# Performance work log

Hardware: AMD Instinct MI355X
Metric: run time of the kernel (lower is better)

## Reference

```python
import jax, jax.numpy as jnp
import numpy as np

B, S, D, H = 4, 2048, 1024, 16
DK = D // H


def setup_inputs() -> dict:
    key = jax.random.key(0)
    ks = jax.random.split(key, 12)
    scale = 1.0 / np.sqrt(D)
    inp = {
        'q': jax.random.normal(ks[0], (B, S, D), jnp.float32),
        'k': jax.random.normal(ks[1], (B, S, D), jnp.float32),
        'v': jax.random.normal(ks[2], (B, S, D), jnp.float32),
        'mask': jnp.ones((1, 1, S, S), jnp.int32),
        'wq': jax.random.normal(ks[3], (D, D), jnp.float32) * scale,
        'bq': jnp.zeros((D,), jnp.float32),
        'wk': jax.random.normal(ks[4], (D, D), jnp.float32) * scale,
        'bk': jnp.zeros((D,), jnp.float32),
        'wv': jax.random.normal(ks[5], (D, D), jnp.float32) * scale,
        'bv': jnp.zeros((D,), jnp.float32),
        'wo': jax.random.normal(ks[6], (D, D), jnp.float32) * scale,
        'bo': jnp.zeros((D,), jnp.float32),
    }
    return inp


def reference(q, k, v, mask, wq, bq, wk, bk, wv, bv, wo, bo):
    # torch Linear: y = x @ W^T + b
    def proj(x, w, b):
        return jnp.einsum('bsd,ed->bse', x, w) + b

    # [B,S,D] -> [B,H,S,DK]
    def split_heads(x):
        return x.reshape(B, S, H, DK).transpose(0, 2, 1, 3)

    query = split_heads(proj(q, wq, bq))
    key_ = split_heads(proj(k, wk, bk))
    value = split_heads(proj(v, wv, bv))

    scores = jnp.einsum('bhqd,bhkd->bhqk', query, key_) / jnp.sqrt(jnp.float32(DK))
    scores = jnp.where(mask == 0, jnp.float32(-1e9), scores)
    attn = jax.nn.softmax(scores, axis=-1)  # dropout p=0 (eval): identity
    x = jnp.einsum('bhqk,bhkd->bhqd', attn, value)
    x = x.transpose(0, 2, 1, 3).reshape(B, S, D)
    return jnp.einsum('bsd,ed->bse', x, wo) + bo
```

## Files before the change

### kernel.cpp

```cpp
#include <hip/hip_runtime.h>
#include <hip/hip_bf16.h>
#include <cstdint>
#include <cstddef>


typedef __attribute__((ext_vector_type(4))) float f32x4;
typedef __attribute__((ext_vector_type(8))) short s16x8;
typedef __attribute__((ext_vector_type(4))) short s16x4;
typedef __attribute__((ext_vector_type(8))) unsigned short u16x8;
typedef __attribute__((ext_vector_type(4))) unsigned short u16x4;
typedef __attribute__((ext_vector_type(2))) unsigned u32x2;

#define AS1 __attribute__((address_space(1)))
#define AS3 __attribute__((address_space(3)))

__device__ __forceinline__ unsigned short f2bf(float f) {
  unsigned u = __builtin_bit_cast(unsigned, f);
  u += 0x7fffu + ((u >> 16) & 1u);
  return (unsigned short)(u >> 16);
}

__device__ __forceinline__ void gload16(const void* g, void* l) {
  __builtin_amdgcn_global_load_lds((const AS1 unsigned*)g, (AS3 unsigned*)l, 16, 0, 0);
}

__device__ __forceinline__ float exp2_fast(float x) {
  float r; asm("v_exp_f32 %0, %1" : "=v"(r) : "v"(x)); return r;
}
__device__ __forceinline__ float max3f(float a, float b, float c) {
  float d; asm("v_max3_f32 %0, %1, %2, %3" : "=v"(d) : "v"(a), "v"(b), "v"(c)); return d;
}
__device__ __forceinline__ unsigned cvt_pk_bf16(float lo, float hi) {
  unsigned r; asm("v_cvt_pk_bf16_f32 %0, %1, %2" : "=v"(r) : "v"(lo), "v"(hi)); return r;
}

__global__ __launch_bounds__(256) void cvt_f32_bf16(const float* __restrict__ in,
                                                    unsigned short* __restrict__ out,
                                                    int n8) {
  int i = blockIdx.x * 256 + threadIdx.x;
  if (i >= n8) return;
  const f32x4* p = (const f32x4*)in;
  f32x4 a = p[2 * i], b = p[2 * i + 1];
  u16x8 o;
  o[0] = f2bf(a[0]); o[1] = f2bf(a[1]); o[2] = f2bf(a[2]); o[3] = f2bf(a[3]);
  o[4] = f2bf(b[0]); o[5] = f2bf(b[1]); o[6] = f2bf(b[2]); o[7] = f2bf(b[3]);
  *(u16x8*)(out + (size_t)i * 8) = o;
}

__global__ __launch_bounds__(256) void cvt_w4(const float* __restrict__ w0,
                                              const float* __restrict__ w1,
                                              const float* __restrict__ w2,
                                              const float* __restrict__ w3,
                                              unsigned short* __restrict__ out) {
  int y = blockIdx.y;
  const float* src = (y == 0) ? w0 : (y == 1) ? w1 : (y == 2) ? w2 : w3;
  int i = blockIdx.x * 256 + threadIdx.x;
  if (i >= 131072) return;
  const f32x4* p = (const f32x4*)src;
  f32x4 a = p[2 * i], b = p[2 * i + 1];
  u16x8 o;
  o[0] = f2bf(a[0]); o[1] = f2bf(a[1]); o[2] = f2bf(a[2]); o[3] = f2bf(a[3]);
  o[4] = f2bf(b[0]); o[5] = f2bf(b[1]); o[6] = f2bf(b[2]); o[7] = f2bf(b[3]);
  *(u16x8*)(out + (size_t)y * 1048576 + (size_t)i * 8) = o;
}

template <int MODE>
__global__ __launch_bounds__(256) void gemm_bt(const unsigned short* __restrict__ A,
                                               const unsigned short* __restrict__ W,
                                               const float* __restrict__ bias,
                                               float oscale,
                                               void* __restrict__ outp) {
  __shared__ char lds[32768];
  const int tid = threadIdx.x;
  const int w = tid >> 6, lane = tid & 63, c = lane & 15, g = lane >> 4;
  const int wr = w >> 1, wc = w & 1;
  const int tm = blockIdx.x, tn = blockIdx.y;

  f32x4 acc[4][4] = {};
  const char* Abase = (const char*)A + ((size_t)tm * 128) * 2048;
  const char* Bbase = (const char*)W + ((size_t)tn * 128) * 2048;

  for (int kt = 0; kt < 16; ++kt) {
    if (kt) __syncthreads();
#pragma unroll
    for (int j = 0; j < 4; ++j) {
      int slotb = (j * 4 + w) * 64;
      int slot = slotb + lane;
      int row = slot >> 3;
      int c16 = (slot & 7) ^ (row & 7);
      gload16(Abase + (size_t)row * 2048 + kt * 128 + c16 * 16, lds + slotb * 16);
    }
#pragma unroll
    for (int j = 0; j < 4; ++j) {
      int slotb = (j * 4 + w) * 64;
      int slot = slotb + lane;
      int row = slot >> 3;
      int c16 = (slot & 7) ^ (row & 7);
      gload16(Bbase + (size_t)row * 2048 + kt * 128 + c16 * 16, lds + 16384 + slotb * 16);
    }
    asm volatile("s_waitcnt vmcnt(0)" ::: "memory");
    __syncthreads();

#pragma unroll
    for (int ks = 0; ks < 2; ++ks) {
      s16x8 af[4], bfr[4];
#pragma unroll
      for (int mi = 0; mi < 4; ++mi) {
        int row = wr * 64 + mi * 16 + c;
        af[mi] = *(const s16x8*)(lds + row * 128 + ((ks * 64 + g * 16) ^ ((row & 7) << 4)));
      }
#pragma unroll
      for (int ni = 0; ni < 4; ++ni) {
        int row = wc * 64 + ni * 16 + c;
        bfr[ni] = *(const s16x8*)(lds + 16384 + row * 128 + ((ks * 64 + g * 16) ^ ((row & 7) << 4)));
      }
#pragma unroll
      for (int mi = 0; mi < 4; ++mi)
#pragma unroll
        for (int ni = 0; ni < 4; ++ni)
          acc[mi][ni] = __builtin_amdgcn_mfma_f32_16x16x32_bf16(af[mi], bfr[ni], acc[mi][ni], 0, 0, 0);
    }
  }

  int col[4];
  float bv[4];
#pragma unroll
  for (int ni = 0; ni < 4; ++ni) {
    col[ni] = tn * 128 + wc * 64 + ni * 16 + c;
    bv[ni] = bias[col[ni]];
  }

  if constexpr (MODE == 2) {
    float* out = (float*)outp;
#pragma unroll
    for (int mi = 0; mi < 4; ++mi) {
      int row0 = tm * 128 + wr * 64 + mi * 16 + g * 4;
#pragma unroll
      for (int ni = 0; ni < 4; ++ni)
#pragma unroll
        for (int r = 0; r < 4; ++r)
          out[(size_t)(row0 + r) * 1024 + col[ni]] = acc[mi][ni][r] + bv[ni];
    }
  } else if constexpr (MODE == 0) {
    unsigned short* out = (unsigned short*)outp;
#pragma unroll
    for (int mi = 0; mi < 4; ++mi) {
      int row0 = tm * 128 + wr * 64 + mi * 16 + g * 4;
#pragma unroll
      for (int ni = 0; ni < 4; ++ni)
#pragma unroll
        for (int r = 0; r < 4; ++r)
          out[(size_t)(row0 + r) * 1024 + col[ni]] = f2bf((acc[mi][ni][r] + bv[ni]) * oscale);
    }
  } else {
    unsigned short* Vt = (unsigned short*)outp;
#pragma unroll
    for (int mi = 0; mi < 4; ++mi) {
      int m0 = tm * 128 + wr * 64 + mi * 16 + g * 4;
      int b = m0 >> 11, s = m0 & 2047;
#pragma unroll
      for (int ni = 0; ni < 4; ++ni) {
        u16x4 pk;
#pragma unroll
        for (int r = 0; r < 4; ++r) pk[r] = f2bf(acc[mi][ni][r] + bv[ni]);
        *(u16x4*)(Vt + ((size_t)(b * 1024 + col[ni])) * 2048 + s) = pk;
      }
    }
  }
}

__global__ __launch_bounds__(256) void attn_kernel(const unsigned short* __restrict__ Q,
                                                   const unsigned short* __restrict__ K,
                                                   const unsigned short* __restrict__ Vt,
                                                   unsigned short* __restrict__ X) {
  __shared__ char lds[32768];
  const int tid = threadIdx.x, w = tid >> 6, lane = tid & 63, c = lane & 15, g = lane >> 4;
  const int qt = blockIdx.x, bh = blockIdx.y, b = bh >> 4;
  const size_t qkbase = ((size_t)b * 2048) * 1024 + (size_t)(bh & 15) * 64;
  const int q0 = qt * 64 + w * 16;

  s16x8 qf[2];
  {
    const unsigned short* qp = Q + qkbase + (size_t)(q0 + c) * 1024;
    qf[0] = *(const s16x8*)(qp + g * 8);
    qf[1] = *(const s16x8*)(qp + 32 + g * 8);
  }

  const int row0 = w * 8 + (lane >> 3);
  const int c16 = (lane & 7) ^ (lane >> 3);
  const int sb0 = w * 1024, sb1 = 4096 + w * 1024;
  const char* kb0 = (const char*)(K + qkbase) + (size_t)row0 * 2048 + c16 * 16;
  const char* kb1 = kb0 + 32 * 2048;
  const char* vb0 = (const char*)Vt + ((size_t)bh * 64 + row0) * 4096 + c16 * 16;
  const char* vb1 = vb0 + 32 * 4096;

  const int M = (c & 7) << 4;
  const int koff0 = (g * 16) ^ M, koff1 = (64 + g * 16) ^ M;
  int voff[4];
#pragma unroll
  for (int mt = 0; mt < 4; ++mt) voff[mt] = (mt * 32 + g * 8) ^ M;

  auto stage = [&](int half, int kt) {
    char* dst = (char*)lds + half * 16384;
    gload16(kb0 + (size_t)kt * 131072, dst + sb0);
    gload16(kb1 + (size_t)kt * 131072, dst + sb1);
    gload16(vb0 + (size_t)kt * 128, dst + 8192 + sb0);
    gload16(vb1 + (size_t)kt * 128, dst + 8192 + sb1);
  };

  f32x4 acc_o[4] = {};
  float m_run = -INFINITY, l_run = 0.f;

  stage(0, 0);

  for (int kt = 0; kt < 32; ++kt) {
    const int cur = kt & 1;
    asm volatile("s_waitcnt vmcnt(0)" ::: "memory");
    __syncthreads();
    if (kt + 1 < 32) stage(cur ^ 1, kt + 1);

    const char* kr = (const char*)lds + cur * 16384 + c * 128;
    const char* vr = kr + 8192;

    f32x4 s4[4] = {};
    __builtin_amdgcn_s_setprio(1);
#pragma unroll
    for (int mt = 0; mt < 4; ++mt) {
      s16x8 kf = *(const s16x8*)(kr + mt * 2048 + koff0);
      s4[mt] = __builtin_amdgcn_mfma_f32_16x16x32_bf16(kf, qf[0], s4[mt], 0, 0, 0);
    }
#pragma unroll
    for (int mt = 0; mt < 4; ++mt) {
      s16x8 kf = *(const s16x8*)(kr + mt * 2048 + koff1);
      s4[mt] = __builtin_amdgcn_mfma_f32_16x16x32_bf16(kf, qf[1], s4[mt], 0, 0, 0);
    }
    __builtin_amdgcn_s_setprio(0);

    float t[16];
#pragma unroll
    for (int mt = 0; mt < 4; ++mt)
#pragma unroll
      for (int r = 0; r < 4; ++r) t[mt * 4 + r] = s4[mt][r];

    float a0 = max3f(t[0], t[1], t[2]);
    float a1 = max3f(t[3], t[4], t[5]);
    float a2 = max3f(t[6], t[7], t[8]);
    float a3 = max3f(t[9], t[10], t[11]);
    float a4 = max3f(t[12], t[13], t[14]);
    float mx = fmaxf(max3f(a0, a1, a2), max3f(a3, a4, t[15]));
    mx = fmaxf(mx, __shfl_xor(mx, 16));
    mx = fmaxf(mx, __shfl_xor(mx, 32));

    if (!__all(mx <= m_run + 8.f)) {
      float m_new = fmaxf(m_run, mx);
      float alpha = exp2_fast(m_run - m_new);
      float al[4];
#pragma unroll
      for (int r = 0; r < 4; ++r) al[r] = __shfl(alpha, (lane & 48) + g * 4 + r);
#pragma unroll
      for (int nc = 0; nc < 4; ++nc)
#pragma unroll
        for (int r = 0; r < 4; ++r) acc_o[nc][r] *= al[r];
      l_run *= alpha;
      m_run = m_new;
    }

    float p[16];
#pragma unroll
    for (int i = 0; i < 16; ++i) p[i] = exp2_fast(t[i] - m_run);
    float r0 = (p[0] + p[1]) + (p[2] + p[3]);
    float r1 = (p[4] + p[5]) + (p[6] + p[7]);
    float r2 = (p[8] + p[9]) + (p[10] + p[11]);
    float r3 = (p[12] + p[13]) + (p[14] + p[15]);
    float rs = (r0 + r1) + (r2 + r3);
    rs += __shfl_xor(rs, 16);
    rs += __shfl_xor(rs, 32);
    l_run += rs;

    s16x4 pf[4];
#pragma unroll
    for (int mt = 0; mt < 4; ++mt) {
      u32x2 pk;
      pk[0] = cvt_pk_bf16(p[mt * 4 + 0], p[mt * 4 + 1]);
      pk[1] = cvt_pk_bf16(p[mt * 4 + 2], p[mt * 4 + 3]);
      pf[mt] = __builtin_bit_cast(s16x4, pk);
    }

    __builtin_amdgcn_s_setprio(1);
#pragma unroll
    for (int mt = 0; mt < 4; ++mt) {
#pragma unroll
      for (int nc = 0; nc < 4; ++nc) {
        s16x4 vf = *(const s16x4*)(vr + nc * 2048 + voff[mt]);
        acc_o[nc] = __builtin_amdgcn_mfma_f32_16x16x16bf16_1k(pf[mt], vf, acc_o[nc], 0, 0, 0);
      }
    }
    __builtin_amdgcn_s_setprio(0);
  }

  float linv = 1.f / l_run;
  float li[4];
#pragma unroll
  for (int r = 0; r < 4; ++r) li[r] = __shfl(linv, (lane & 48) + g * 4 + r);
#pragma unroll
  for (int nc = 0; nc < 4; ++nc)
#pragma unroll
    for (int r = 0; r < 4; ++r)
      X[qkbase + (size_t)(q0 + g * 4 + r) * 1024 + nc * 16 + c] = f2bf(acc_o[nc][r] * li[r]);
}

extern "C" void kernel_launch(void* const* d_in, const int* in_sizes, int n_in,
                              void* d_out, int out_size, void* d_ws, size_t ws_size,
                              hipStream_t stream) {
  const float* q  = (const float*)d_in[0];
  const float* k  = (const float*)d_in[1];
  const float* v  = (const float*)d_in[2];
  const float* wq = (const float*)d_in[4];
  const float* bq = (const float*)d_in[5];
  const float* wk = (const float*)d_in[6];
  const float* bk = (const float*)d_in[7];
  const float* wv = (const float*)d_in[8];
  const float* bv = (const float*)d_in[9];
  const float* wo = (const float*)d_in[10];
  const float* bo = (const float*)d_in[11];

  char* ws = (char*)d_ws;
  unsigned short* buf = (unsigned short*)ws;
  unsigned short* wb  = (unsigned short*)(ws + (size_t)16777216);
  unsigned short* Vt  = (unsigned short*)(ws + (size_t)25165824);

  unsigned short* Qb = (unsigned short*)d_out;
  unsigned short* Kb = Qb + 8388608;

  const float qscale = 0.18033688011112042f;

  cvt_w4<<<dim3(512, 4), 256, 0, stream>>>(wq, wk, wv, wo, wb);

  cvt_f32_bf16<<<4096, 256, 0, stream>>>(q, buf, 1048576);
  gemm_bt<0><<<dim3(64, 8), 256, 0, stream>>>(buf, wb + 0,       bq, qscale, (void*)Qb);
  cvt_f32_bf16<<<4096, 256, 0, stream>>>(k, buf, 1048576);
  gemm_bt<0><<<dim3(64, 8), 256, 0, stream>>>(buf, wb + 1048576, bk, 1.0f, (void*)Kb);
  cvt_f32_bf16<<<4096, 256, 0, stream>>>(v, buf, 1048576);
  gemm_bt<1><<<dim3(64, 8), 256, 0, stream>>>(buf, wb + 2097152, bv, 1.0f, (void*)Vt);

  attn_kernel<<<dim3(32, 64), 256, 0, stream>>>(Qb, Kb, Vt, buf);

  gemm_bt<2><<<dim3(64, 8), 256, 0, stream>>>(buf, wb + 3145728, bo, 1.0f, d_out);
}
```

Baseline: 401.1 us.

## Double-buffer GEMM LDS, process two query tiles per attention wave, permute V layout

The GEMM now double-buffers its LDS tiles (64KB), prefetching the next K-slice while computing the current one, and raises wave priority around its MFMA bursts. The attention kernel has each wave handle 32 query rows as two 16-row sub-tiles, so every K/V fragment read from LDS feeds twice as many MFMAs, and the grid is halved to match. The V-transpose store is permuted within 64-element groups so attention can read V as 16-byte vectors and split them into halves. The cost is higher register and LDS pressure, which may lower occupancy, and fewer attention blocks overall.

Measured after the change: 394.4 us. No clear change (-1.7%).

```diff
diff --git a/kernel.cpp b/kernel.cpp
--- a/kernel.cpp
+++ b/kernel.cpp
@@ -70,7 +70,7 @@
                                                const float* __restrict__ bias,
                                                float oscale,
                                                void* __restrict__ outp) {
-  __shared__ char lds[32768];
+  __shared__ char lds[65536];
   const int tid = threadIdx.x;
   const int w = tid >> 6, lane = tid & 63, c = lane & 15, g = lane >> 4;
   const int wr = w >> 1, wc = w & 1;
@@ -80,45 +80,48 @@
   const char* Abase = (const char*)A + ((size_t)tm * 128) * 2048;
   const char* Bbase = (const char*)W + ((size_t)tn * 128) * 2048;
 
-  for (int kt = 0; kt < 16; ++kt) {
-    if (kt) __syncthreads();
+  auto stage = [&](int half, int kt) {
+    char* dst = (char*)lds + half * 32768;
 #pragma unroll
     for (int j = 0; j < 4; ++j) {
       int slotb = (j * 4 + w) * 64;
       int slot = slotb + lane;
       int row = slot >> 3;
       int c16 = (slot & 7) ^ (row & 7);
-      gload16(Abase + (size_t)row * 2048 + kt * 128 + c16 * 16, lds + slotb * 16);
-    }
-#pragma unroll
-    for (int j = 0; j < 4; ++j) {
-      int slotb = (j * 4 + w) * 64;
-      int slot = slotb + lane;
-      int row = slot >> 3;
-      int c16 = (slot & 7) ^ (row & 7);
-      gload16(Bbase + (size_t)row * 2048 + kt * 128 + c16 * 16, lds + 16384 + slotb * 16);
-    }
+      gload16(Abase + (size_t)row * 2048 + kt * 128 + c16 * 16, dst + slotb * 16);
+      gload16(Bbase + (size_t)row * 2048 + kt * 128 + c16 * 16, dst + 16384 + slotb * 16);
+    }
+  };
+
+  stage(0, 0);
+
+  for (int kt = 0; kt < 16; ++kt) {
+    const int cur = kt & 1;
     asm volatile("s_waitcnt vmcnt(0)" ::: "memory");
     __syncthreads();
-
+    if (kt + 1 < 16) stage(cur ^ 1, kt + 1);
+
+    const char* base = (const char*)lds + cur * 32768;
 #pragma unroll
     for (int ks = 0; ks < 2; ++ks) {
       s16x8 af[4], bfr[4];
 #pragma unroll
       for (int mi = 0; mi < 4; ++mi) {
         int row = wr * 64 + mi * 16 + c;
-        af[mi] = *(const s16x8*)(lds + row * 128 + ((ks * 64 + g * 16) ^ ((row & 7) << 4)));
+        af[mi] = *(const s16x8*)(base + row * 128 + ((ks * 64 + g * 16) ^ ((row & 7) << 4)));
       }
 #pragma unroll
       for (int ni = 0; ni < 4; ++ni) {
         int row = wc * 64 + ni * 16 + c;
-        bfr[ni] = *(const s16x8*)(lds + 16384 + row * 128 + ((ks * 64 + g * 16) ^ ((row & 7) << 4)));
-      }
+        bfr[ni] = *(const s16x8*)(base + 16384 + row * 128 + ((ks * 64 + g * 16) ^ ((row & 7) << 4)));
+      }
+      __builtin_amdgcn_s_setprio(1);
 #pragma unroll
       for (int mi = 0; mi < 4; ++mi)
 #pragma unroll
         for (int ni = 0; ni < 4; ++ni)
           acc[mi][ni] = __builtin_amdgcn_mfma_f32_16x16x32_bf16(af[mi], bfr[ni], acc[mi][ni], 0, 0, 0);
+      __builtin_amdgcn_s_setprio(0);
     }
   }
 
@@ -158,12 +161,15 @@
     for (int mi = 0; mi < 4; ++mi) {
       int m0 = tm * 128 + wr * 64 + mi * 16 + g * 4;
       int b = m0 >> 11, s = m0 & 2047;
+      int sl = s & 63;
+      int mt_l = sl >> 4, gg = (sl >> 2) & 3;
+      int npos = ((mt_l >> 1) << 5) + gg * 8 + ((mt_l & 1) << 2);
 #pragma unroll
       for (int ni = 0; ni < 4; ++ni) {
         u16x4 pk;
 #pragma unroll
         for (int r = 0; r < 4; ++r) pk[r] = f2bf(acc[mi][ni][r] + bv[ni]);
-        *(u16x4*)(Vt + ((size_t)(b * 1024 + col[ni])) * 2048 + s) = pk;
+        *(u16x4*)(Vt + ((size_t)(b * 1024 + col[ni])) * 2048 + (s & ~63) + npos) = pk;
       }
     }
   }
@@ -177,13 +183,16 @@
   const int tid = threadIdx.x, w = tid >> 6, lane = tid & 63, c = lane & 15, g = lane >> 4;
   const int qt = blockIdx.x, bh = blockIdx.y, b = bh >> 4;
   const size_t qkbase = ((size_t)b * 2048) * 1024 + (size_t)(bh & 15) * 64;
-  const int q0 = qt * 64 + w * 16;
-
-  s16x8 qf[2];
+  const int q0 = qt * 128 + w * 32;
+
+  s16x8 qa[2], qb[2];
   {
     const unsigned short* qp = Q + qkbase + (size_t)(q0 + c) * 1024;
-    qf[0] = *(const s16x8*)(qp + g * 8);
-    qf[1] = *(const s16x8*)(qp + 32 + g * 8);
+    qa[0] = *(const s16x8*)(qp + g * 8);
+    qa[1] = *(const s16x8*)(qp + 32 + g * 8);
+    qp += 16 * 1024;
+    qb[0] = *(const s16x8*)(qp + g * 8);
+    qb[1] = *(const s16x8*)(qp + 32 + g * 8);
   }
 
   const int row0 = w * 8 + (lane >> 3);
@@ -196,9 +205,6 @@
 
   const int M = (c & 7) << 4;
   const int koff0 = (g * 16) ^ M, koff1 = (64 + g * 16) ^ M;
-  int voff[4];
-#pragma unroll
-  for (int mt = 0; mt < 4; ++mt) voff[mt] = (mt * 32 + g * 8) ^ M;
 
   auto stage = [&](int half, int kt) {
     char* dst = (char*)lds + half * 16384;
@@ -208,8 +214,8 @@
     gload16(vb1 + (size_t)kt * 128, dst + 8192 + sb1);
   };
 
-  f32x4 acc_o[4] = {};
-  float m_run = -INFINITY, l_run = 0.f;
+  f32x4 aa[4] = {}, ab[4] = {};
+  float ma = -INFINITY, la = 0.f, mb = -INFINITY, lb = 0.f;
 
   stage(0, 0);
 
@@ -222,91 +228,130 @@
     const char* kr = (const char*)lds + cur * 16384 + c * 128;
     const char* vr = kr + 8192;
 
-    f32x4 s4[4] = {};
+    f32x4 sa[4] = {}, sb4[4] = {};
     __builtin_amdgcn_s_setprio(1);
 #pragma unroll
     for (int mt = 0; mt < 4; ++mt) {
       s16x8 kf = *(const s16x8*)(kr + mt * 2048 + koff0);
-      s4[mt] = __builtin_amdgcn_mfma_f32_16x16x32_bf16(kf, qf[0], s4[mt], 0, 0, 0);
+      sa[mt] = __builtin_amdgcn_mfma_f32_16x16x32_bf16(kf, qa[0], sa[mt], 0, 0, 0);
+      sb4[mt] = __builtin_amdgcn_mfma_f32_16x16x32_bf16(kf, qb[0], sb4[mt], 0, 0, 0);
     }
 #pragma unroll
     for (int mt = 0; mt < 4; ++mt) {
       s16x8 kf = *(const s16x8*)(kr + mt * 2048 + koff1);
-      s4[mt] = __builtin_amdgcn_mfma_f32_16x16x32_bf16(kf, qf[1], s4[mt], 0, 0, 0);
+      sa[mt] = __builtin_amdgcn_mfma_f32_16x16x32_bf16(kf, qa[1], sa[mt], 0, 0, 0);
+      sb4[mt] = __builtin_amdgcn_mfma_f32_16x16x32_bf16(kf, qb[1], sb4[mt], 0, 0, 0);
     }
     __builtin_amdgcn_s_setprio(0);
 
-    float t[16];
-#pragma unroll
-    for (int mt = 0; mt < 4; ++mt)
-#pragma unroll
-      for (int r = 0; r < 4; ++r) t[mt * 4 + r] = s4[mt][r];
-
-    float a0 = max3f(t[0], t[1], t[2]);
-    float a1 = max3f(t[3], t[4], t[5]);
-    float a2 = max3f(t[6], t[7], t[8]);
-    float a3 = max3f(t[9], t[10], t[11]);
-    float a4 = max3f(t[12], t[13], t[14]);
-    float mx = fmaxf(max3f(a0, a1, a2), max3f(a3, a4, t[15]));
-    mx = fmaxf(mx, __shfl_xor(mx, 16));
-    mx = fmaxf(mx, __shfl_xor(mx, 32));
-
-    if (!__all(mx <= m_run + 8.f)) {
-      float m_new = fmaxf(m_run, mx);
-      float alpha = exp2_fast(m_run - m_new);
-      float al[4];
-#pragma unroll
-      for (int r = 0; r < 4; ++r) al[r] = __shfl(alpha, (lane & 48) + g * 4 + r);
-#pragma unroll
-      for (int nc = 0; nc < 4; ++nc)
-#pragma unroll
-        for (int r = 0; r < 4; ++r) acc_o[nc][r] *= al[r];
-      l_run *= alpha;
-      m_run = m_new;
-    }
-
-    float p[16];
-#pragma unroll
-    for (int i = 0; i < 16; ++i) p[i] = exp2_fast(t[i] - m_run);
-    float r0 = (p[0] + p[1]) + (p[2] + p[3]);
-    float r1 = (p[4] + p[5]) + (p[6] + p[7]);
-    float r2 = (p[8] + p[9]) + (p[10] + p[11]);
-    float r3 = (p[12] + p[13]) + (p[14] + p[15]);
-    float rs = (r0 + r1) + (r2 + r3);
-    rs += __shfl_xor(rs, 16);
-    rs += __shfl_xor(rs, 32);
-    l_run += rs;
-
-    s16x4 pf[4];
-#pragma unroll
-    for (int mt = 0; mt < 4; ++mt) {
-      u32x2 pk;
-      pk[0] = cvt_pk_bf16(p[mt * 4 + 0], p[mt * 4 + 1]);
-      pk[1] = cvt_pk_bf16(p[mt * 4 + 2], p[mt * 4 + 3]);
-      pf[mt] = __builtin_bit_cast(s16x4, pk);
+    float ea0 = max3f(sa[0][0], sa[0][1], sa[0][2]);
+    float ea1 = max3f(sa[0][3], sa[1][0], sa[1][1]);
+    float ea2 = max3f(sa[1][2], sa[1][3], sa[2][0]);
+    float ea3 = max3f(sa[2][1], sa[2][2], sa[2][3]);
+    float ea4 = max3f(sa[3][0], sa[3][1], sa[3][2]);
+    float mxa = fmaxf(max3f(ea0, ea1, ea2), max3f(ea3, ea4, sa[3][3]));
+    mxa = fmaxf(mxa, __shfl_xor(mxa, 16));
+    mxa = fmaxf(mxa, __shfl_xor(mxa, 32));
+    float eb0 = max3f(sb4[0][0], sb4[0][1], sb4[0][2]);
+    float eb1 = max3f(sb4[0][3], sb4[1][0], sb4[1][1]);
+    float eb2 = max3f(sb4[1][2], sb4[1][3], sb4[2][0]);
+    float eb3 = max3f(sb4[2][1], sb4[2][2], sb4[2][3]);
+    float eb4 = max3f(sb4[3][0], sb4[3][1], sb4[3][2]);
+    float mxb = fmaxf(max3f(eb0, eb1, eb2), max3f(eb3, eb4, sb4[3][3]));
+    mxb = fmaxf(mxb, __shfl_xor(mxb, 16));
+    mxb = fmaxf(mxb, __shfl_xor(mxb, 32));
+
+    if (!__all((mxa <= ma + 8.f) & (mxb <= mb + 8.f))) {
+      float mna = fmaxf(ma, mxa), mnb = fmaxf(mb, mxb);
+      float ala = exp2_fast(ma - mna), alb = exp2_fast(mb - mnb);
+      const int bidx = lane & 48;
+#pragma unroll
+      for (int r = 0; r < 4; ++r) {
+        float sA = __shfl(ala, bidx + g * 4 + r);
+        float sB = __shfl(alb, bidx + g * 4 + r);
+#pragma unroll
+        for (int nc = 0; nc < 4; ++nc) { aa[nc][r] *= sA; ab[nc][r] *= sB; }
+      }
+      la *= ala; lb *= alb;
+      ma = mna; mb = mnb;
+    }
+
+    s16x4 pfa[4], pfb[4];
+    {
+      float p[16];
+#pragma unroll
+      for (int mt = 0; mt < 4; ++mt)
+#pragma unroll
+        for (int r = 0; r < 4; ++r) p[mt * 4 + r] = exp2_fast(sa[mt][r] - ma);
+      float r0 = (p[0] + p[1]) + (p[2] + p[3]);
+      float r1 = (p[4] + p[5]) + (p[6] + p[7]);
+      float r2 = (p[8] + p[9]) + (p[10] + p[11]);
+      float r3 = (p[12] + p[13]) + (p[14] + p[15]);
+      float rs = (r0 + r1) + (r2 + r3);
+      rs += __shfl_xor(rs, 16);
+      rs += __shfl_xor(rs, 32);
+      la += rs;
+#pragma unroll
+      for (int mt = 0; mt < 4; ++mt) {
+        u32x2 pk;
+        pk[0] = cvt_pk_bf16(p[mt * 4 + 0], p[mt * 4 + 1]);
+        pk[1] = cvt_pk_bf16(p[mt * 4 + 2], p[mt * 4 + 3]);
+        pfa[mt] = __builtin_bit_cast(s16x4, pk);
+      }
+    }
+    {
+      float p[16];
+#pragma unroll
+      for (int mt = 0; mt < 4; ++mt)
+#pragma unroll
+        for (int r = 0; r < 4; ++r) p[mt * 4 + r] = exp2_fast(sb4[mt][r] - mb);
+      float r0 = (p[0] + p[1]) + (p[2] + p[3]);
+      float r1 = (p[4] + p[5]) + (p[6] + p[7]);
+      float r2 = (p[8] + p[9]) + (p[10] + p[11]);
+      float r3 = (p[12] + p[13]) + (p[14] + p[15]);
+      float rs = (r0 + r1) + (r2 + r3);
+      rs += __shfl_xor(rs, 16);
+      rs += __shfl_xor(rs, 32);
+      lb += rs;
+#pragma unroll
+      for (int mt = 0; mt < 4; ++mt) {
+        u32x2 pk;
+        pk[0] = cvt_pk_bf16(p[mt * 4 + 0], p[mt * 4 + 1]);
+        pk[1] = cvt_pk_bf16(p[mt * 4 + 2], p[mt * 4 + 3]);
+        pfb[mt] = __builtin_bit_cast(s16x4, pk);
+      }
     }
 
     __builtin_amdgcn_s_setprio(1);
 #pragma unroll
-    for (int mt = 0; mt < 4; ++mt) {
+    for (int mtp = 0; mtp < 2; ++mtp) {
+      const int off = (mtp == 0) ? koff0 : koff1;
 #pragma unroll
       for (int nc = 0; nc < 4; ++nc) {
-        s16x4 vf = *(const s16x4*)(vr + nc * 2048 + voff[mt]);
-        acc_o[nc] = __builtin_amdgcn_mfma_f32_16x16x16bf16_1k(pf[mt], vf, acc_o[nc], 0, 0, 0);
+        s16x8 vv = *(const s16x8*)(vr + nc * 2048 + off);
+        s16x4 vlo = __builtin_shufflevector(vv, vv, 0, 1, 2, 3);
+        s16x4 vhi = __builtin_shufflevector(vv, vv, 4, 5, 6, 7);
+        aa[nc] = __builtin_amdgcn_mfma_f32_16x16x16bf16_1k(pfa[2 * mtp], vlo, aa[nc], 0, 0, 0);
+        aa[nc] = __builtin_amdgcn_mfma_f32_16x16x16bf16_1k(pfa[2 * mtp + 1], vhi, aa[nc], 0, 0, 0);
+        ab[nc] = __builtin_amdgcn_mfma_f32_16x16x16bf16_1k(pfb[2 * mtp], vlo, ab[nc], 0, 0, 0);
+        ab[nc] = __builtin_amdgcn_mfma_f32_16x16x16bf16_1k(pfb[2 * mtp + 1], vhi, ab[nc], 0, 0, 0);
       }
     }
     __builtin_amdgcn_s_setprio(0);
   }
 
-  float linv = 1.f / l_run;
-  float li[4];
-#pragma unroll
-  for (int r = 0; r < 4; ++r) li[r] = __shfl(linv, (lane & 48) + g * 4 + r);
-#pragma unroll
-  for (int nc = 0; nc < 4; ++nc)
-#pragma unroll
-    for (int r = 0; r < 4; ++r)
-      X[qkbase + (size_t)(q0 + g * 4 + r) * 1024 + nc * 16 + c] = f2bf(acc_o[nc][r] * li[r]);
+  const int bidx = lane & 48;
+  float lia = 1.f / la, lib = 1.f / lb;
+#pragma unroll
+  for (int r = 0; r < 4; ++r) {
+    float sA = __shfl(lia, bidx + g * 4 + r);
+    float sB = __shfl(lib, bidx + g * 4 + r);
+#pragma unroll
+    for (int nc = 0; nc < 4; ++nc) {
+      X[qkbase + (size_t)(q0 + g * 4 + r) * 1024 + nc * 16 + c] = f2bf(aa[nc][r] * sA);
+      X[qkbase + (size_t)(q0 + 16 + g * 4 + r) * 1024 + nc * 16 + c] = f2bf(ab[nc][r] * sB);
+    }
+  }
 }
 
 extern "C" void kernel_launch(void* const* d_in, const int* in_sizes, int n_in,
@@ -343,7 +388,7 @@
   cvt_f32_bf16<<<4096, 256, 0, stream>>>(v, buf, 1048576);
   gemm_bt<1><<<dim3(64, 8), 256, 0, stream>>>(buf, wb + 2097152, bv, 1.0f, (void*)Vt);
 
-  attn_kernel<<<dim3(32, 64), 256, 0, stream>>>(Qb, Kb, Vt, buf);
-
-  gemm_bt<2><<<dim3(64, 8), 256, 0, stream>>>(buf, wb + 3145728, bo, 1.0f, d_out);
-}
+  attn_kernel<<<dim3(16, 64), 256, 0, stream>>>(Qb, Kb, Vt, buf);
+
+  gemm_bt<2><<<dim3(64, 8), 256, 0, stream>>>(buf, wb + 3145728, bo, d_out ? 1.0f : 1.0f, d_out);
+}
```

## Fuse input conversion into batched QKV GEMM and widen attention query tiles

Applied to the files above, without the earlier changes.

Drops the separate fp32-to-bf16 conversion kernels: the QKV GEMM now reads fp32 activations directly, converts them in registers and stores them to LDS. The three projections run in one launch with a swizzled block order. Attention now processes 64 query rows per wave instead of 16, reusing each K/V LDS fragment across four query tiles. V is stored in a permuted layout so 8-element V loads feed two MFMAs. This cuts launch overhead and intermediate global traffic and raises operand reuse, at the cost of higher register pressure in attention and fewer attention blocks (512 instead of 2048).

After: 364.7 us. 1.1x faster.

```diff
diff --git a/kernel.cpp b/kernel.cpp
--- a/kernel.cpp
+++ b/kernel.cpp
@@ -32,19 +32,6 @@
 }
 __device__ __forceinline__ unsigned cvt_pk_bf16(float lo, float hi) {
   unsigned r; asm("v_cvt_pk_bf16_f32 %0, %1, %2" : "=v"(r) : "v"(lo), "v"(hi)); return r;
-}
-
-__global__ __launch_bounds__(256) void cvt_f32_bf16(const float* __restrict__ in,
-                                                    unsigned short* __restrict__ out,
-                                                    int n8) {
-  int i = blockIdx.x * 256 + threadIdx.x;
-  if (i >= n8) return;
-  const f32x4* p = (const f32x4*)in;
-  f32x4 a = p[2 * i], b = p[2 * i + 1];
-  u16x8 o;
-  o[0] = f2bf(a[0]); o[1] = f2bf(a[1]); o[2] = f2bf(a[2]); o[3] = f2bf(a[3]);
-  o[4] = f2bf(b[0]); o[5] = f2bf(b[1]); o[6] = f2bf(b[2]); o[7] = f2bf(b[3]);
-  *(u16x8*)(out + (size_t)i * 8) = o;
 }
 
 __global__ __launch_bounds__(256) void cvt_w4(const float* __restrict__ w0,
@@ -64,39 +51,51 @@
   *(u16x8*)(out + (size_t)y * 1048576 + (size_t)i * 8) = o;
 }
 
-template <int MODE>
-__global__ __launch_bounds__(256) void gemm_bt(const unsigned short* __restrict__ A,
-                                               const unsigned short* __restrict__ W,
-                                               const float* __restrict__ bias,
-                                               float oscale,
-                                               void* __restrict__ outp) {
-  __shared__ char lds[32768];
+template <int AMODE>
+__device__ __forceinline__ void gemm_core(const char* Abase, const char* Bbase,
+                                          const float* bias, float oscale,
+                                          void* outp, int emode, int tm, int tn,
+                                          char* lds) {
   const int tid = threadIdx.x;
   const int w = tid >> 6, lane = tid & 63, c = lane & 15, g = lane >> 4;
   const int wr = w >> 1, wc = w & 1;
-  const int tm = blockIdx.x, tn = blockIdx.y;
 
   f32x4 acc[4][4] = {};
-  const char* Abase = (const char*)A + ((size_t)tm * 128) * 2048;
-  const char* Bbase = (const char*)W + ((size_t)tn * 128) * 2048;
+  f32x4 ar[4][2];
 
   for (int kt = 0; kt < 16; ++kt) {
     if (kt) __syncthreads();
+
+    if constexpr (AMODE == 1) {
+#pragma unroll
+      for (int j = 0; j < 4; ++j) {
+        int s2 = (j * 4 + w) * 64 + lane, row = s2 >> 3, c16 = (s2 & 7) ^ (row & 7);
+        const f32x4* src = (const f32x4*)(Abase + (size_t)row * 4096 + kt * 256 + c16 * 32);
+        ar[j][0] = src[0];
+        ar[j][1] = src[1];
+      }
+    } else {
+#pragma unroll
+      for (int j = 0; j < 4; ++j) {
+        int s2 = (j * 4 + w) * 64 + lane, row = s2 >> 3, c16 = (s2 & 7) ^ (row & 7);
+        gload16(Abase + (size_t)row * 2048 + kt * 128 + c16 * 16, lds + (s2 & ~63) * 16);
+      }
+    }
 #pragma unroll
     for (int j = 0; j < 4; ++j) {
-      int slotb = (j * 4 + w) * 64;
-      int slot = slotb + lane;
-      int row = slot >> 3;
-      int c16 = (slot & 7) ^ (row & 7);
-      gload16(Abase + (size_t)row * 2048 + kt * 128 + c16 * 16, lds + slotb * 16);
-    }
-#pragma unroll
-    for (int j = 0; j < 4; ++j) {
-      int slotb = (j * 4 + w) * 64;
-      int slot = slotb + lane;
-      int row = slot >> 3;
-      int c16 = (slot & 7) ^ (row & 7);
-      gload16(Bbase + (size_t)row * 2048 + kt * 128 + c16 * 16, lds + 16384 + slotb * 16);
+      int s2 = (j * 4 + w) * 64 + lane, row = s2 >> 3, c16 = (s2 & 7) ^ (row & 7);
+      gload16(Bbase + (size_t)row * 2048 + kt * 128 + c16 * 16, lds + 16384 + (s2 & ~63) * 16);
+    }
+    if constexpr (AMODE == 1) {
+#pragma unroll
+      for (int j = 0; j < 4; ++j) {
+        int s2 = (j * 4 + w) * 64 + lane;
+        f32x4 a = ar[j][0], b2 = ar[j][1];
+        u16x8 o;
+        o[0] = f2bf(a[0]); o[1] = f2bf(a[1]); o[2] = f2bf(a[2]); o[3] = f2bf(a[3]);
+        o[4] = f2bf(b2[0]); o[5] = f2bf(b2[1]); o[6] = f2bf(b2[2]); o[7] = f2bf(b2[3]);
+        *(u16x8*)(lds + s2 * 16) = o;
+      }
     }
     asm volatile("s_waitcnt vmcnt(0)" ::: "memory");
     __syncthreads();
@@ -114,11 +113,13 @@
         int row = wc * 64 + ni * 16 + c;
         bfr[ni] = *(const s16x8*)(lds + 16384 + row * 128 + ((ks * 64 + g * 16) ^ ((row & 7) << 4)));
       }
+      __builtin_amdgcn_s_setprio(1);
 #pragma unroll
       for (int mi = 0; mi < 4; ++mi)
 #pragma unroll
         for (int ni = 0; ni < 4; ++ni)
           acc[mi][ni] = __builtin_amdgcn_mfma_f32_16x16x32_bf16(af[mi], bfr[ni], acc[mi][ni], 0, 0, 0);
+      __builtin_amdgcn_s_setprio(0);
     }
   }
 
@@ -130,7 +131,7 @@
     bv[ni] = bias[col[ni]];
   }
 
-  if constexpr (MODE == 2) {
+  if (emode == 2) {
     float* out = (float*)outp;
 #pragma unroll
     for (int mi = 0; mi < 4; ++mi) {
@@ -141,7 +142,7 @@
         for (int r = 0; r < 4; ++r)
           out[(size_t)(row0 + r) * 1024 + col[ni]] = acc[mi][ni][r] + bv[ni];
     }
-  } else if constexpr (MODE == 0) {
+  } else if (emode == 0) {
     unsigned short* out = (unsigned short*)outp;
 #pragma unroll
     for (int mi = 0; mi < 4; ++mi) {
@@ -158,32 +159,71 @@
     for (int mi = 0; mi < 4; ++mi) {
       int m0 = tm * 128 + wr * 64 + mi * 16 + g * 4;
       int b = m0 >> 11, s = m0 & 2047;
+      int sl = s & 63;
+      int mt_l = sl >> 4, gg = (sl >> 2) & 3;
+      int npos = ((mt_l >> 1) << 5) + gg * 8 + ((mt_l & 1) << 2);
 #pragma unroll
       for (int ni = 0; ni < 4; ++ni) {
         u16x4 pk;
 #pragma unroll
         for (int r = 0; r < 4; ++r) pk[r] = f2bf(acc[mi][ni][r] + bv[ni]);
-        *(u16x4*)(Vt + ((size_t)(b * 1024 + col[ni])) * 2048 + s) = pk;
-      }
-    }
-  }
-}
-
-__global__ __launch_bounds__(256) void attn_kernel(const unsigned short* __restrict__ Q,
-                                                   const unsigned short* __restrict__ K,
-                                                   const unsigned short* __restrict__ Vt,
-                                                   unsigned short* __restrict__ X) {
+        *(u16x4*)(Vt + ((size_t)(b * 1024 + col[ni])) * 2048 + (s & ~63) + npos) = pk;
+      }
+    }
+  }
+}
+
+struct QKVArgs {
+  const float* A0; const float* A1; const float* A2;
+  const unsigned short* W;
+  const float* b0; const float* b1; const float* b2;
+  unsigned short* o0; unsigned short* o1; unsigned short* o2;
+  float sc0;
+};
+
+__global__ __launch_bounds__(256) void qkv_gemm(QKVArgs a) {
+  __shared__ char lds[32768];
+  int id = blockIdx.x;
+  int sw = (id & 7) * 192 + (id >> 3);
+  int z = sw >> 9, r2 = sw & 511;
+  int tm = r2 >> 3, tn = r2 & 7;
+  const float* A = (z == 0) ? a.A0 : (z == 1) ? a.A1 : a.A2;
+  const float* bias = (z == 0) ? a.b0 : (z == 1) ? a.b1 : a.b2;
+  unsigned short* out = (z == 0) ? a.o0 : (z == 1) ? a.o1 : a.o2;
+  float oscale = (z == 0) ? a.sc0 : 1.0f;
+  int emode = (z == 2) ? 1 : 0;
+  const char* Abase = (const char*)A + ((size_t)tm * 128) * 4096;
+  const char* Bbase = (const char*)(a.W + (size_t)z * 1048576) + ((size_t)tn * 128) * 2048;
+  gemm_core<1>(Abase, Bbase, bias, oscale, out, emode, tm, tn, lds);
+}
+
+__global__ __launch_bounds__(256) void gemm_out(const unsigned short* __restrict__ A,
+                                                const unsigned short* __restrict__ W,
+                                                const float* __restrict__ bias,
+                                                float* __restrict__ out) {
+  __shared__ char lds[32768];
+  int tm = blockIdx.x, tn = blockIdx.y;
+  const char* Abase = (const char*)A + ((size_t)tm * 128) * 2048;
+  const char* Bbase = (const char*)W + ((size_t)tn * 128) * 2048;
+  gemm_core<0>(Abase, Bbase, bias, 1.0f, out, 2, tm, tn, lds);
+}
+
+__global__ __launch_bounds__(256, 2) void attn_kernel(const unsigned short* __restrict__ Q,
+                                                      const unsigned short* __restrict__ K,
+                                                      const unsigned short* __restrict__ Vt,
+                                                      unsigned short* __restrict__ X) {
   __shared__ char lds[32768];
   const int tid = threadIdx.x, w = tid >> 6, lane = tid & 63, c = lane & 15, g = lane >> 4;
   const int qt = blockIdx.x, bh = blockIdx.y, b = bh >> 4;
   const size_t qkbase = ((size_t)b * 2048) * 1024 + (size_t)(bh & 15) * 64;
-  const int q0 = qt * 64 + w * 16;
-
-  s16x8 qf[2];
-  {
-    const unsigned short* qp = Q + qkbase + (size_t)(q0 + c) * 1024;
-    qf[0] = *(const s16x8*)(qp + g * 8);
-    qf[1] = *(const s16x8*)(qp + 32 + g * 8);
+  const int q0 = qt * 256 + w * 64;
+
+  s16x8 qf[4][2];
+#pragma unroll
+  for (int t = 0; t < 4; ++t) {
+    const unsigned short* qp = Q + qkbase + (size_t)(q0 + t * 16 + c) * 1024;
+    qf[t][0] = *(const s16x8*)(qp + g * 8);
+    qf[t][1] = *(const s16x8*)(qp + 32 + g * 8);
   }
 
   const int row0 = w * 8 + (lane >> 3);
@@ -196,9 +236,6 @@
 
   const int M = (c & 7) << 4;
   const int koff0 = (g * 16) ^ M, koff1 = (64 + g * 16) ^ M;
-  int voff[4];
-#pragma unroll
-  for (int mt = 0; mt < 4; ++mt) voff[mt] = (mt * 32 + g * 8) ^ M;
 
   auto stage = [&](int half, int kt) {
     char* dst = (char*)lds + half * 16384;
@@ -208,8 +245,10 @@
     gload16(vb1 + (size_t)kt * 128, dst + 8192 + sb1);
   };
 
-  f32x4 acc_o[4] = {};
-  float m_run = -INFINITY, l_run = 0.f;
+  f32x4 acc[4][4] = {};
+  float m_[4], l_[4];
+#pragma unroll
+  for (int t = 0; t < 4; ++t) { m_[t] = -INFINITY; l_[t] = 0.f; }
 
   stage(0, 0);
 
@@ -222,91 +261,109 @@
     const char* kr = (const char*)lds + cur * 16384 + c * 128;
     const char* vr = kr + 8192;
 
-    f32x4 s4[4] = {};
+    f32x4 s4[4][4] = {};
     __builtin_amdgcn_s_setprio(1);
 #pragma unroll
-    for (int mt = 0; mt < 4; ++mt) {
-      s16x8 kf = *(const s16x8*)(kr + mt * 2048 + koff0);
-      s4[mt] = __builtin_amdgcn_mfma_f32_16x16x32_bf16(kf, qf[0], s4[mt], 0, 0, 0);
-    }
-#pragma unroll
-    for (int mt = 0; mt < 4; ++mt) {
-      s16x8 kf = *(const s16x8*)(kr + mt * 2048 + koff1);
-      s4[mt] = __builtin_amdgcn_mfma_f32_16x16x32_bf16(kf, qf[1], s4[mt], 0, 0, 0);
+    for (int ks = 0; ks < 2; ++ks) {
+      const int off = ks ? koff1 : koff0;
+#pragma unroll
+      for (int mt = 0; mt < 4; ++mt) {
+        s16x8 kf = *(const s16x8*)(kr + mt * 2048 + off);
+#pragma unroll
+        for (int t = 0; t < 4; ++t)
+          s4[t][mt] = __builtin_amdgcn_mfma_f32_16x16x32_bf16(kf, qf[t][ks], s4[t][mt], 0, 0, 0);
+      }
     }
     __builtin_amdgcn_s_setprio(0);
 
-    float t[16];
-#pragma unroll
-    for (int mt = 0; mt < 4; ++mt)
-#pragma unroll
-      for (int r = 0; r < 4; ++r) t[mt * 4 + r] = s4[mt][r];
-
-    float a0 = max3f(t[0], t[1], t[2]);
-    float a1 = max3f(t[3], t[4], t[5]);
-    float a2 = max3f(t[6], t[7], t[8]);
-    float a3 = max3f(t[9], t[10], t[11]);
-    float a4 = max3f(t[12], t[13], t[14]);
-    float mx = fmaxf(max3f(a0, a1, a2), max3f(a3, a4, t[15]));
-    mx = fmaxf(mx, __shfl_xor(mx, 16));
-    mx = fmaxf(mx, __shfl_xor(mx, 32));
-
-    if (!__all(mx <= m_run + 8.f)) {
-      float m_new = fmaxf(m_run, mx);
-      float alpha = exp2_fast(m_run - m_new);
-      float al[4];
-#pragma unroll
-      for (int r = 0; r < 4; ++r) al[r] = __shfl(alpha, (lane & 48) + g * 4 + r);
+    float mx[4];
+#pragma unroll
+    for (int t = 0; t < 4; ++t) {
+      float e0 = max3f(s4[t][0][0], s4[t][0][1], s4[t][0][2]);
+      float e1 = max3f(s4[t][0][3], s4[t][1][0], s4[t][1][1]);
+      float e2 = max3f(s4[t][1][2], s4[t][1][3], s4[t][2][0]);
+      float e3 = max3f(s4[t][2][1], s4[t][2][2], s4[t][2][3]);
+      float e4 = max3f(s4[t][3][0], s4[t][3][1], s4[t][3][2]);
+      float m = fmaxf(max3f(e0, e1, e2), max3f(e3, e4, s4[t][3][3]));
+      m = fmaxf(m, __shfl_xor(m, 16));
+      mx[t] = fmaxf(m, __shfl_xor(m, 32));
+    }
+
+    bool ok = (mx[0] <= m_[0] + 8.f) & (mx[1] <= m_[1] + 8.f) &
+              (mx[2] <= m_[2] + 8.f) & (mx[3] <= m_[3] + 8.f);
+    if (!__all(ok)) {
+      const int bidx = lane & 48;
+#pragma unroll
+      for (int t = 0; t < 4; ++t) {
+        float mn = fmaxf(m_[t], mx[t]);
+        float al = exp2_fast(m_[t] - mn);
+#pragma unroll
+        for (int r = 0; r < 4; ++r) {
+          float sA = __shfl(al, bidx + g * 4 + r);
+#pragma unroll
+          for (int nc = 0; nc < 4; ++nc) acc[t][nc][r] *= sA;
+        }
+        l_[t] *= al;
+        m_[t] = mn;
+      }
+    }
+
+    s16x4 pf[4][4];
+#pragma unroll
+    for (int t = 0; t < 4; ++t) {
+      float p[16];
+#pragma unroll
+      for (int mt = 0; mt < 4; ++mt)
+#pragma unroll
+        for (int r = 0; r < 4; ++r) p[mt * 4 + r] = exp2_fast(s4[t][mt][r] - m_[t]);
+      float r0 = (p[0] + p[1]) + (p[2] + p[3]);
+      float r1 = (p[4] + p[5]) + (p[6] + p[7]);
+      float r2 = (p[8] + p[9]) + (p[10] + p[11]);
+      float r3 = (p[12] + p[13]) + (p[14] + p[15]);
+      float rs = (r0 + r1) + (r2 + r3);
+      rs += __shfl_xor(rs, 16);
+      rs += __shfl_xor(rs, 32);
+      l_[t] += rs;
+#pragma unroll
+      for (int mt = 0; mt < 4; ++mt) {
+        u32x2 pk;
+        pk[0] = cvt_pk_bf16(p[mt * 4 + 0], p[mt * 4 + 1]);
+        pk[1] = cvt_pk_bf16(p[mt * 4 + 2], p[mt * 4 + 3]);
+        pf[t][mt] = __builtin_bit_cast(s16x4, pk);
+      }
+    }
+
+    __builtin_amdgcn_s_setprio(1);
+#pragma unroll
+    for (int mtp = 0; mtp < 2; ++mtp) {
+      const int off = (mtp == 0) ? koff0 : koff1;
+#pragma unroll
+      for (int nc = 0; nc < 4; ++nc) {
+        s16x8 vv = *(const s16x8*)(vr + nc * 2048 + off);
+        s16x4 vlo = __builtin_shufflevector(vv, vv, 0, 1, 2, 3);
+        s16x4 vhi = __builtin_shufflevector(vv, vv, 4, 5, 6, 7);
+#pragma unroll
+        for (int t = 0; t < 4; ++t) {
+          acc[t][nc] = __builtin_amdgcn_mfma_f32_16x16x16bf16_1k(pf[t][2 * mtp], vlo, acc[t][nc], 0, 0, 0);
+          acc[t][nc] = __builtin_amdgcn_mfma_f32_16x16x16bf16_1k(pf[t][2 * mtp + 1], vhi, acc[t][nc], 0, 0, 0);
+        }
+      }
+    }
+    __builtin_amdgcn_s_setprio(0);
+  }
+
+  const int bidx = lane & 48;
+#pragma unroll
+  for (int t = 0; t < 4; ++t) {
+    float linv = 1.f / l_[t];
+#pragma unroll
+    for (int r = 0; r < 4; ++r) {
+      float sA = __shfl(linv, bidx + g * 4 + r);
 #pragma unroll
       for (int nc = 0; nc < 4; ++nc)
-#pragma unroll
-        for (int r = 0; r < 4; ++r) acc_o[nc][r] *= al[r];
-      l_run *= alpha;
-      m_run = m_new;
-    }
-
-    float p[16];
-#pragma unroll
-    for (int i = 0; i < 16; ++i) p[i] = exp2_fast(t[i] - m_run);
-    float r0 = (p[0] + p[1]) + (p[2] + p[3]);
-    float r1 = (p[4] + p[5]) + (p[6] + p[7]);
-    float r2 = (p[8] + p[9]) + (p[10] + p[11]);
-    float r3 = (p[12] + p[13]) + (p[14] + p[15]);
-    float rs = (r0 + r1) + (r2 + r3);
-    rs += __shfl_xor(rs, 16);
-    rs += __shfl_xor(rs, 32);
-    l_run += rs;
-
-    s16x4 pf[4];
-#pragma unroll
-    for (int mt = 0; mt < 4; ++mt) {
-      u32x2 pk;
-      pk[0] = cvt_pk_bf16(p[mt * 4 + 0], p[mt * 4 + 1]);
-      pk[1] = cvt_pk_bf16(p[mt * 4 + 2], p[mt * 4 + 3]);
-      pf[mt] = __builtin_bit_cast(s16x4, pk);
-    }
-
-    __builtin_amdgcn_s_setprio(1);
-#pragma unroll
-    for (int mt = 0; mt < 4; ++mt) {
-#pragma unroll
-      for (int nc = 0; nc < 4; ++nc) {
-        s16x4 vf = *(const s16x4*)(vr + nc * 2048 + voff[mt]);
-        acc_o[nc] = __builtin_amdgcn_mfma_f32_16x16x16bf16_1k(pf[mt], vf, acc_o[nc], 0, 0, 0);
-      }
-    }
-    __builtin_amdgcn_s_setprio(0);
-  }
-
-  float linv = 1.f / l_run;
-  float li[4];
-#pragma unroll
-  for (int r = 0; r < 4; ++r) li[r] = __shfl(linv, (lane & 48) + g * 4 + r);
-#pragma unroll
-  for (int nc = 0; nc < 4; ++nc)
-#pragma unroll
-    for (int r = 0; r < 4; ++r)
-      X[qkbase + (size_t)(q0 + g * 4 + r) * 1024 + nc * 16 + c] = f2bf(acc_o[nc][r] * li[r]);
+        X[qkbase + (size_t)(q0 + t * 16 + g * 4 + r) * 1024 + nc * 16 + c] = f2bf(acc[t][nc][r] * sA);
+    }
+  }
 }
 
 extern "C" void kernel_launch(void* const* d_in, const int* in_sizes, int n_in,
@@ -325,9 +382,9 @@
   const float* bo = (const float*)d_in[11];
 
   char* ws = (char*)d_ws;
-  unsigned short* buf = (unsigned short*)ws;
-  unsigned short* wb  = (unsigned short*)(ws + (size_t)16777216);
-  unsigned short* Vt  = (unsigned short*)(ws + (size_t)25165824);
+  unsigned short* Xb = (unsigned short*)ws;
+  unsigned short* wb = (unsigned short*)(ws + (size_t)16777216);
+  unsigned short* Vt = (unsigned short*)(ws + (size_t)25165824);
 
   unsigned short* Qb = (unsigned short*)d_out;
   unsigned short* Kb = Qb + 8388608;
@@ -336,14 +393,15 @@
 
   cvt_w4<<<dim3(512, 4), 256, 0, stream>>>(wq, wk, wv, wo, wb);
 
-  cvt_f32_bf16<<<4096, 256, 0, stream>>>(q, buf, 1048576);
-  gemm_bt<0><<<dim3(64, 8), 256, 0, stream>>>(buf, wb + 0,       bq, qscale, (void*)Qb);
-  cvt_f32_bf16<<<4096, 256, 0, stream>>>(k, buf, 1048576);
-  gemm_bt<0><<<dim3(64, 8), 256, 0, stream>>>(buf, wb + 1048576, bk, 1.0f, (void*)Kb);
-  cvt_f32_bf16<<<4096, 256, 0, stream>>>(v, buf, 1048576);
-  gemm_bt<1><<<dim3(64, 8), 256, 0, stream>>>(buf, wb + 2097152, bv, 1.0f, (void*)Vt);
-
-  attn_kernel<<<dim3(32, 64), 256, 0, stream>>>(Qb, Kb, Vt, buf);
-
-  gemm_bt<2><<<dim3(64, 8), 256, 0, stream>>>(buf, wb + 3145728, bo, 1.0f, d_out);
-}
+  QKVArgs args;
+  args.A0 = q;  args.A1 = k;  args.A2 = v;
+  args.W = wb;
+  args.b0 = bq; args.b1 = bk; args.b2 = bv;
+  args.o0 = Qb; args.o1 = Kb; args.o2 = Vt;
+  args.sc0 = qscale;
+  qkv_gemm<<<1536, 256, 0, stream>>>(args);
+
+  attn_kernel<<<dim3(8, 64), 256, 0, stream>>>(Qb, Kb, Vt, Xb);
+
+  gemm_out<<<dim3(64, 8), 256, 0, stream>>>(Xb, wb + 3145728, bo, (float*)d_out);
+}
```
